# Optimization experiments

Hardware: AMD Instinct MI355X
Metric: run time of the kernel (lower is better)

The kernel has to match this reference:

```python
import jax, jax.numpy as jnp
import numpy as np

N_NODES = 50000
N_EDGES = 800000
IN_C, HID_C, OUT_C = 128, 128, 64


def setup_inputs() -> dict:
    key = jax.random.key(0)
    k1, k2, k3, k4 = jax.random.split(key, 4)
    x = jax.random.normal(k1, (N_NODES, IN_C), dtype=jnp.float32)
    edge_index = jax.random.randint(k2, (2, N_EDGES), 0, N_NODES, dtype=jnp.int64)
    # Glorot-ish init for weights, zero bias (PyG GCNConv default has bias)
    W1 = jax.random.normal(k3, (IN_C, HID_C), dtype=jnp.float32) * (1.0 / np.sqrt(IN_C))
    b1 = jnp.zeros((HID_C,), dtype=jnp.float32)
    W2 = jax.random.normal(k4, (HID_C, OUT_C), dtype=jnp.float32) * (1.0 / np.sqrt(HID_C))
    b2 = jnp.zeros((OUT_C,), dtype=jnp.float32)
    return {"x": x, "edge_index": edge_index, "W1": W1, "b1": b1, "W2": W2, "b2": b2}


def _gcn_norm(edge_index, num_nodes):
    """PyG gcn_norm: add self-loops, symmetric deg^{-1/2} normalization."""
    loop = jnp.arange(num_nodes, dtype=edge_index.dtype)
    src = jnp.concatenate([edge_index[0], loop])  # [E + N]
    dst = jnp.concatenate([edge_index[1], loop])
    ones = jnp.ones(src.shape[0], dtype=jnp.float32)
    deg = jax.ops.segment_sum(ones, dst, num_segments=num_nodes)  # in-degree incl. self-loop
    dinv = jnp.where(deg > 0, jax.lax.rsqrt(deg), 0.0)
    norm = dinv[src] * dinv[dst]  # [E + N]
    return src, dst, norm


def _gcn_conv(x, W, b, src, dst, norm, num_nodes):
    h = x @ W                                   # [N, C_out] transform first (PyG order)
    msg = h[src] * norm[:, None]                # gather + normalize, [E+N, C_out]
    out = jax.ops.segment_sum(msg, dst, num_segments=num_nodes)  # scatter-add
    return out + b


def reference(x, edge_index, W1, b1, W2, b2):
    N = x.shape[0]
    src, dst, norm = _gcn_norm(edge_index, N)  # graph normalization shared by both layers
    h = jax.nn.relu(_gcn_conv(x, W1, b1, src, dst, norm, N))
    out = _gcn_conv(h, W2, b2, src, dst, norm, N)
    return out
```

## Files before the change

### kernel.cpp

```cpp
#include <hip/hip_runtime.h>
#include <hip/hip_bf16.h>

#define IN_C  128
#define HID_C 128
#define OUT_CC 64
#define BK    128
#define CAPLG 12

using short8  = __attribute__((ext_vector_type(8))) short;
using float4v = __attribute__((ext_vector_type(4))) float;

__device__ __forceinline__ unsigned short f2b(float f) {
    unsigned int u = __float_as_uint(f);
    return (unsigned short)((u + 0x7fffu + ((u >> 16) & 1u)) >> 16);
}
__device__ __forceinline__ unsigned int pack2(float a, float b) {
    return (unsigned int)f2b(a) | ((unsigned int)f2b(b) << 16);
}
__device__ __forceinline__ float2 bf2_to_f2(unsigned int v) {
    float2 r;
    r.x = __uint_as_float(v << 16);
    r.y = __uint_as_float(v & 0xffff0000u);
    return r;
}


__global__ __launch_bounds__(256) void k_bpart(const int* __restrict__ ei,
                                               int* __restrict__ bfill,
                                               int* __restrict__ ebuf, int E, int NBK,
                                               int NCHK,
                                               const float* __restrict__ W1,
                                               const float* __restrict__ W2,
                                               unsigned short* __restrict__ w1f,
                                               unsigned short* __restrict__ w2f) {
    const int t = threadIdx.x;
    if ((int)blockIdx.x >= NCHK) {
        int e = ((int)blockIdx.x - NCHK) * 256 + t;
        if (e < 16384) {
            int j = e & 7, lane = (e >> 3) & 63, ks = (e >> 9) & 3, nt = e >> 11;
            int k = ks * 32 + ((lane >> 4) << 3) + j;
            int n = nt * 16 + (lane & 15);
            w1f[e] = f2b(W1[k * 128 + n]);
        } else if (e < 16384 + 8192) {
            int e2 = e - 16384;
            int j = e2 & 7, lane = (e2 >> 3) & 63, ks = (e2 >> 9) & 3, nt = e2 >> 11;
            int k = ks * 32 + ((lane >> 4) << 3) + j;
            int n = nt * 16 + (lane & 15);
            w2f[e2] = f2b(W2[k * 64 + n]);
        }
        return;
    }
    __shared__ int lh[512];
    __shared__ int lbase[512];
    __shared__ int s_st;
    for (int i = t; i < NBK; i += 256) lh[i] = 0;
    if (t < 64) {
        int ev = ei[2 * t], od = ei[2 * t + 1];
        unsigned long long onz = __ballot(od != 0);
        unsigned long long enz = __ballot(ev != 0);
        if (t == 0) s_st = (onz == 0ull && enz != 0ull) ? 2 : 1;
    }
    __syncthreads();
    const int st = s_st;
    const int base = blockIdx.x * 2048;
    int s[8], d[8];
    #pragma unroll
    for (int j = 0; j < 8; ++j) {
        int i = base + j * 256 + t;
        if (i < E) {
            s[j] = ei[(size_t)st * i];
            d[j] = ei[(size_t)st * ((size_t)E + i)];
            atomicAdd(&lh[d[j] >> 7], 1);
        } else d[j] = -1;
    }
    __syncthreads();
    for (int i = t; i < NBK; i += 256) {
        int c = lh[i];
        lbase[i] = c ? atomicAdd(&bfill[i], c) : 0;
        lh[i] = 0;
    }
    __syncthreads();
    #pragma unroll
    for (int j = 0; j < 8; ++j) {
        if (d[j] >= 0) {
            int b = d[j] >> 7;
            int r = lbase[b] + atomicAdd(&lh[b], 1);
            if (r < (1 << CAPLG))
                ebuf[(b << CAPLG) + r] = s[j] | ((d[j] & (BK - 1)) << 20);
        }
    }
}

__global__ __launch_bounds__(256) void k_blmg1(const int* __restrict__ ebuf,
                                               const int* __restrict__ bfill,
                                               int2* __restrict__ begend,
                                               float* __restrict__ dinv,
                                               int* __restrict__ col,
                                               const float* __restrict__ x,
                                               const unsigned short* __restrict__ w1f,
                                               unsigned short* __restrict__ h,
                                               int N, int NBK) {
    __shared__ unsigned short lds[64 * 136];
    __shared__ int cnt64[64];
    const int t = threadIdx.x;

    if ((int)blockIdx.x < NBK) {
        int* cnt = (int*)lds;
        int* sc  = cnt + BK;
        int* off = sc + BK;
        const int n0 = blockIdx.x * BK;
        const int beg = (int)blockIdx.x << CAPLG;
        const int ecnt = min(bfill[blockIdx.x], 1 << CAPLG);
        if (t < BK) cnt[t] = 0;
        __syncthreads();
        for (int i = t; i < ecnt; i += 256)
            atomicAdd(&cnt[ebuf[beg + i] >> 20], 1);
        __syncthreads();
        if (t < BK) sc[t] = cnt[t];
        __syncthreads();
        for (int o = 1; o < BK; o <<= 1) {
            int v = (t < BK && t >= o) ? sc[t - o] : 0;
            __syncthreads();
            if (t < BK) sc[t] += v;
            __syncthreads();
        }
        if (t < BK) {
            int c = cnt[t];
            off[t] = sc[t] - c;
            if (n0 + t < N) {
                begend[n0 + t] = make_int2(beg + off[t], beg + sc[t]);
                dinv[n0 + t] = rsqrtf((float)c + 1.0f);
            }
            cnt[t] = 0;
        }
        __syncthreads();
        for (int i = t; i < ecnt; i += 256) {
            int e = ebuf[beg + i];
            int dl = e >> 20;
            int p = beg + off[dl] + atomicAdd(&cnt[dl], 1);
            col[p] = e & 0xFFFFF;
        }
        return;
    }

    const int tile = (int)blockIdx.x - NBK;
    const int row0 = tile * 64;
    const int bkt  = row0 >> 7;
    const int half = (row0 >> 6) & 1;
    if (t < 64) cnt64[t] = 0;
    __syncthreads();
    {
        const int ebeg = bkt << CAPLG;
        const int ecnt = min(bfill[bkt], 1 << CAPLG);
        for (int i = t; i < ecnt; i += 256) {
            int dl = ebuf[ebeg + i] >> 20;
            if ((dl >> 6) == half) atomicAdd(&cnt64[dl & 63], 1);
        }
    }
    {
        int r = t >> 2, cc = (t & 3) * 32;
        int grow = row0 + r;
        unsigned int* dst = (unsigned int*)&lds[r * 136 + cc];
        if (grow < N) {
            const float4* src = (const float4*)(x + (size_t)grow * 128 + cc);
            #pragma unroll
            for (int i = 0; i < 8; ++i) {
                float4 v = src[i];
                dst[2 * i]     = pack2(v.x, v.y);
                dst[2 * i + 1] = pack2(v.z, v.w);
            }
        } else {
            #pragma unroll
            for (int i = 0; i < 16; ++i) dst[i] = 0;
        }
    }
    __syncthreads();
    const int w = t >> 6, lane = t & 63;
    const int quad = lane >> 4, m = lane & 15;
    short8 a[4];
    #pragma unroll
    for (int ks = 0; ks < 4; ++ks)
        a[ks] = *(const short8*)&lds[(w * 16 + m) * 136 + ks * 32 + quad * 8];
    float4v acc[8];
    #pragma unroll
    for (int nt = 0; nt < 8; ++nt) acc[nt] = (float4v){0.f, 0.f, 0.f, 0.f};
    const short8* wf = (const short8*)w1f;
    #pragma unroll
    for (int nt = 0; nt < 8; ++nt)
        #pragma unroll
        for (int ks = 0; ks < 4; ++ks)
            acc[nt] = __builtin_amdgcn_mfma_f32_16x16x32_bf16(a[ks], wf[(nt * 4 + ks) * 64 + lane],
                                                              acc[nt], 0, 0, 0);
    float drr[4];
    #pragma unroll
    for (int r = 0; r < 4; ++r) {
        int lr = w * 16 + quad * 4 + r;
        drr[r] = rsqrtf((float)cnt64[lr] + 1.0f);
    }
    #pragma unroll
    for (int nt = 0; nt < 8; ++nt)
        #pragma unroll
        for (int r = 0; r < 4; ++r) {
            int grow = row0 + w * 16 + quad * 4 + r;
            if (grow < N) h[(size_t)grow * 128 + nt * 16 + m] = f2b(acc[nt][r] * drr[r]);
        }
}

#define ACC16(u) { float2 q; \
    q = bf2_to_f2(u.x); a0 += q.x; a1 += q.y; \
    q = bf2_to_f2(u.y); a2 += q.x; a3 += q.y; \
    q = bf2_to_f2(u.z); a4 += q.x; a5 += q.y; \
    q = bf2_to_f2(u.w); a6 += q.x; a7 += q.y; }

#define PIPE_GATHER(FEATP, ROWSTRIDE, LANEOFF) \
    int c0, c1, c2, c3; \
    uint4 u0, u1, u2, u3; \
    { \
        int rem = end - e; \
        if (rem >= 4) { \
            c0 = col[e]; c1 = col[e + 1]; c2 = col[e + 2]; c3 = col[e + 3]; \
            u0 = FEATP[(size_t)c0 * ROWSTRIDE + LANEOFF]; \
            u1 = FEATP[(size_t)c1 * ROWSTRIDE + LANEOFF]; \
            u2 = FEATP[(size_t)c2 * ROWSTRIDE + LANEOFF]; \
            u3 = FEATP[(size_t)c3 * ROWSTRIDE + LANEOFF]; \
            if (rem >= 8) { c0 = col[e + 4]; c1 = col[e + 5]; c2 = col[e + 6]; c3 = col[e + 7]; } \
        } \
    } \
    for (; e + 12 <= end; e += 4) { \
        int n0 = col[e + 8], n1 = col[e + 9], n2 = col[e + 10], n3 = col[e + 11]; \
        uint4 v0 = FEATP[(size_t)c0 * ROWSTRIDE + LANEOFF]; \
        uint4 v1 = FEATP[(size_t)c1 * ROWSTRIDE + LANEOFF]; \
        uint4 v2 = FEATP[(size_t)c2 * ROWSTRIDE + LANEOFF]; \
        uint4 v3 = FEATP[(size_t)c3 * ROWSTRIDE + LANEOFF]; \
        ACC16(u0) ACC16(u1) ACC16(u2) ACC16(u3) \
        u0 = v0; u1 = v1; u2 = v2; u3 = v3; \
        c0 = n0; c1 = n1; c2 = n2; c3 = n3; \
    } \
    if (e + 8 <= end) { \
        uint4 v0 = FEATP[(size_t)c0 * ROWSTRIDE + LANEOFF]; \
        uint4 v1 = FEATP[(size_t)c1 * ROWSTRIDE + LANEOFF]; \
        uint4 v2 = FEATP[(size_t)c2 * ROWSTRIDE + LANEOFF]; \
        uint4 v3 = FEATP[(size_t)c3 * ROWSTRIDE + LANEOFF]; \
        ACC16(u0) ACC16(u1) ACC16(u2) ACC16(u3) \
        ACC16(v0) ACC16(v1) ACC16(v2) ACC16(v3) \
        e += 8; \
    } else if (e + 4 <= end) { \
        ACC16(u0) ACC16(u1) ACC16(u2) ACC16(u3) \
        e += 4; \
    } \
    for (; e < end; ++e) { \
        uint4 u = FEATP[(size_t)col[e] * ROWSTRIDE + LANEOFF]; \
        ACC16(u) \
    }

__global__ __launch_bounds__(256) void k_aggmg2(const uint4* __restrict__ feat,
                                                const int2* __restrict__ begend,
                                                const int* __restrict__ col,
                                                const float* __restrict__ dinv,
                                                const float* __restrict__ b1,
                                                const unsigned short* __restrict__ w2f,
                                                unsigned short* __restrict__ h2, int N) {
    __shared__ unsigned short lds[16 * 136];
    __shared__ float dvs[16];
    const int grp = threadIdx.x >> 4;
    const int l16 = threadIdx.x & 15;
    const int node = blockIdx.x * 16 + grp;
    float a0 = 0.f, a1 = 0.f, a2 = 0.f, a3 = 0.f, a4 = 0.f, a5 = 0.f, a6 = 0.f, a7 = 0.f;
    if (node < N) {
        const float dd = dinv[node];
        if (l16 == 0) dvs[grp] = dd;
        const int2 be = begend[node];
        int e = be.x; const int end = be.y;
        {
            uint4 sv = feat[(size_t)node * 16 + l16];
            float2 q;
            q = bf2_to_f2(sv.x); a0 = q.x; a1 = q.y;
            q = bf2_to_f2(sv.y); a2 = q.x; a3 = q.y;
            q = bf2_to_f2(sv.z); a4 = q.x; a5 = q.y;
            q = bf2_to_f2(sv.w); a6 = q.x; a7 = q.y;
        }
        PIPE_GATHER(feat, 16, l16)
        float4 ba = ((const float4*)b1)[2 * l16];
        float4 bb = ((const float4*)b1)[2 * l16 + 1];
        a0 = fmaxf(a0 * dd + ba.x, 0.0f);
        a1 = fmaxf(a1 * dd + ba.y, 0.0f);
        a2 = fmaxf(a2 * dd + ba.z, 0.0f);
        a3 = fmaxf(a3 * dd + ba.w, 0.0f);
        a4 = fmaxf(a4 * dd + bb.x, 0.0f);
        a5 = fmaxf(a5 * dd + bb.y, 0.0f);
        a6 = fmaxf(a6 * dd + bb.z, 0.0f);
        a7 = fmaxf(a7 * dd + bb.w, 0.0f);
    } else if (l16 == 0) dvs[grp] = 0.f;
    {
        uint4 o;
        o.x = pack2(a0, a1);
        o.y = pack2(a2, a3);
        o.z = pack2(a4, a5);
        o.w = pack2(a6, a7);
        *(uint4*)&lds[grp * 136 + l16 * 8] = o;
    }
    __syncthreads();
    const int w = threadIdx.x >> 6, lane = threadIdx.x & 63;
    const int quad = lane >> 4, m = lane & 15;
    short8 a[4];
    #pragma unroll
    for (int ks = 0; ks < 4; ++ks)
        a[ks] = *(const short8*)&lds[m * 136 + ks * 32 + quad * 8];
    float4v acc = (float4v){0.f, 0.f, 0.f, 0.f};
    const short8* wf = (const short8*)w2f;
    #pragma unroll
    for (int ks = 0; ks < 4; ++ks)
        acc = __builtin_amdgcn_mfma_f32_16x16x32_bf16(a[ks], wf[(w * 4 + ks) * 64 + lane],
                                                      acc, 0, 0, 0);
    const int node0 = blockIdx.x * 16;
    #pragma unroll
    for (int r = 0; r < 4; ++r) {
        int gn = node0 + quad * 4 + r;
        if (gn < N) h2[(size_t)gn * 64 + w * 16 + m] = f2b(acc[r] * dvs[quad * 4 + r]);
    }
}

__global__ __launch_bounds__(256) void k_agg64(const uint4* __restrict__ feat,
                                               const int2* __restrict__ begend,
                                               const int* __restrict__ col,
                                               const float* __restrict__ dinv,
                                               const float* __restrict__ bias,
                                               float* __restrict__ out, int N) {
    const int grp = threadIdx.x >> 3;
    const int l8  = threadIdx.x & 7;
    const int node = blockIdx.x * 32 + grp;
    if (node >= N) return;
    const float dd = dinv[node];
    const int2 be = begend[node];
    int e = be.x; const int end = be.y;
    float a0, a1, a2, a3, a4, a5, a6, a7;
    {
        uint4 sv = feat[(size_t)node * 8 + l8];
        float2 q;
        q = bf2_to_f2(sv.x); a0 = q.x; a1 = q.y;
        q = bf2_to_f2(sv.y); a2 = q.x; a3 = q.y;
        q = bf2_to_f2(sv.z); a4 = q.x; a5 = q.y;
        q = bf2_to_f2(sv.w); a6 = q.x; a7 = q.y;
    }
    PIPE_GATHER(feat, 8, l8)
    float4 ba = ((const float4*)bias)[2 * l8];
    float4 bb = ((const float4*)bias)[2 * l8 + 1];
    float4 o1, o2;
    o1.x = a0 * dd + ba.x;
    o1.y = a1 * dd + ba.y;
    o1.z = a2 * dd + ba.z;
    o1.w = a3 * dd + ba.w;
    o2.x = a4 * dd + bb.x;
    o2.y = a5 * dd + bb.y;
    o2.z = a6 * dd + bb.z;
    o2.w = a7 * dd + bb.w;
    float4* op = (float4*)out + (size_t)node * 16 + 2 * l8;
    op[0] = o1;
    op[1] = o2;
}

extern "C" void kernel_launch(void* const* d_in, const int* in_sizes, int n_in,
                              void* d_out, int out_size, void* d_ws, size_t ws_size,
                              hipStream_t stream) {
    const float* x  = (const float*)d_in[0];
    const int*   ei = (const int*)d_in[1];
    const float* W1 = (const float*)d_in[2];
    const float* b1 = (const float*)d_in[3];
    const float* W2 = (const float*)d_in[4];
    const float* b2 = (const float*)d_in[5];

    const int N = in_sizes[0] / IN_C;
    const int E = in_sizes[1] / 2;
    const int NBK  = (N + BK - 1) / BK;
    const int NCHK = (E + 2047) / 2048;
    const int NT1  = (N + 63) / 64;

    char* ws = (char*)d_ws;
    int*            bfill   = (int*)(ws + 64);
    int2*           begend  = (int2*)(ws + 4096);
    float*          dinv    = (float*)(ws + 404480);
    unsigned short* w1f     = (unsigned short*)(ws + 604672);
    unsigned short* w2f     = (unsigned short*)(ws + 637440);
    int*            ebuf    = (int*)(ws + 655360);
    int*            col     = (int*)(ws + 7061504);
    unsigned short* h       = (unsigned short*)(ws + 13467904);
    unsigned short* h2      = (unsigned short*)(ws + 26267904);

    hipMemsetAsync(bfill, 0, NBK * sizeof(int), stream);

    k_bpart<<<NCHK + 96, 256, 0, stream>>>(ei, bfill, ebuf, E, NBK, NCHK,
                                           W1, W2, w1f, w2f);

    k_blmg1<<<NBK + NT1, 256, 0, stream>>>(ebuf, bfill, begend, dinv, col,
                                           x, w1f, h, N, NBK);

    k_aggmg2<<<(N + 15) / 16, 256, 0, stream>>>((const uint4*)h, begend, col, dinv, b1,
                                                w2f, h2, N);

    k_agg64<<<(N + 31) / 32, 256, 0, stream>>>((const uint4*)h2, begend, col, dinv, b2,
                                               (float*)d_out, N);
}
```

Before: 164.3 us.

## Sort nodes by degree bucket to balance gather work across wavefront groups

Builds a degree histogram in the CSR build kernel, then a new kernel creates a permutation of nodes grouped by (capped) in-degree. Both aggregation kernels iterate nodes through this permutation, so the lanes of one wavefront handle nodes with similar edge counts and lose less time to divergent loop lengths. The gather macro is also simplified to a shallower software pipeline. This costs an extra launch, atomic-based binning, an indirect node lookup and scattered output writes, and row locality in h/h2 reads and writes is lost.

```diff
diff --git a/kernel.cpp b/kernel.cpp
--- a/kernel.cpp
+++ b/kernel.cpp
@@ -99,15 +99,17 @@
                                                const float* __restrict__ x,
                                                const unsigned short* __restrict__ w1f,
                                                unsigned short* __restrict__ h,
+                                               int* __restrict__ gbins,
                                                int N, int NBK) {
     __shared__ unsigned short lds[64 * 136];
     __shared__ int cnt64[64];
     const int t = threadIdx.x;
 
     if ((int)blockIdx.x < NBK) {
-        int* cnt = (int*)lds;
-        int* sc  = cnt + BK;
-        int* off = sc + BK;
+        int* cnt   = (int*)lds;
+        int* sc    = cnt + BK;
+        int* off   = sc + BK;
+        int* lbins = off + BK;
         const int n0 = blockIdx.x * BK;
         const int beg = (int)blockIdx.x << CAPLG;
         const int ecnt = min(bfill[blockIdx.x], 1 << CAPLG);
@@ -124,22 +126,28 @@
             if (t < BK) sc[t] += v;
             __syncthreads();
         }
+        int mydeg = -1;
         if (t < BK) {
             int c = cnt[t];
             off[t] = sc[t] - c;
             if (n0 + t < N) {
                 begend[n0 + t] = make_int2(beg + off[t], beg + sc[t]);
                 dinv[n0 + t] = rsqrtf((float)c + 1.0f);
+                mydeg = min(c, 63);
             }
             cnt[t] = 0;
         }
+        if (t >= 128 && t < 192) lbins[t - 128] = 0;
         __syncthreads();
+        if (mydeg >= 0) atomicAdd(&lbins[mydeg], 1);
         for (int i = t; i < ecnt; i += 256) {
             int e = ebuf[beg + i];
             int dl = e >> 20;
             int p = beg + off[dl] + atomicAdd(&cnt[dl], 1);
             col[p] = e & 0xFFFFF;
         }
+        __syncthreads();
+        if (t < 64 && lbins[t]) atomicAdd(&gbins[t], lbins[t]);
         return;
     }
 
@@ -206,6 +214,27 @@
         }
 }
 
+__global__ __launch_bounds__(128) void k_perm(const int2* __restrict__ begend,
+                                              const int* __restrict__ gbins,
+                                              int* __restrict__ binfill,
+                                              int* __restrict__ perm, int N) {
+    __shared__ int boff[64];
+    const int t = threadIdx.x;
+    if (t == 0) {
+        int s = 0;
+        #pragma unroll
+        for (int i = 0; i < 64; ++i) { int c = gbins[i]; boff[i] = s; s += c; }
+    }
+    __syncthreads();
+    int node = blockIdx.x * 128 + t;
+    if (node < N) {
+        int2 be = begend[node];
+        int dg = min(be.y - be.x, 63);
+        int r = boff[dg] + atomicAdd(&binfill[dg], 1);
+        perm[r] = node;
+    }
+}
+
 #define ACC16(u) { float2 q; \
     q = bf2_to_f2(u.x); a0 += q.x; a1 += q.y; \
     q = bf2_to_f2(u.y); a2 += q.x; a3 += q.y; \
@@ -214,37 +243,21 @@
 
 #define PIPE_GATHER(FEATP, ROWSTRIDE, LANEOFF) \
     int c0, c1, c2, c3; \
-    uint4 u0, u1, u2, u3; \
-    { \
-        int rem = end - e; \
-        if (rem >= 4) { \
-            c0 = col[e]; c1 = col[e + 1]; c2 = col[e + 2]; c3 = col[e + 3]; \
-            u0 = FEATP[(size_t)c0 * ROWSTRIDE + LANEOFF]; \
-            u1 = FEATP[(size_t)c1 * ROWSTRIDE + LANEOFF]; \
-            u2 = FEATP[(size_t)c2 * ROWSTRIDE + LANEOFF]; \
-            u3 = FEATP[(size_t)c3 * ROWSTRIDE + LANEOFF]; \
-            if (rem >= 8) { c0 = col[e + 4]; c1 = col[e + 5]; c2 = col[e + 6]; c3 = col[e + 7]; } \
-        } \
+    if (e + 4 <= end) { c0 = col[e]; c1 = col[e + 1]; c2 = col[e + 2]; c3 = col[e + 3]; } \
+    for (; e + 8 <= end; e += 4) { \
+        int p0 = col[e + 4], p1 = col[e + 5], p2 = col[e + 6], p3 = col[e + 7]; \
+        uint4 u0 = FEATP[(size_t)c0 * ROWSTRIDE + LANEOFF]; \
+        uint4 u1 = FEATP[(size_t)c1 * ROWSTRIDE + LANEOFF]; \
+        uint4 u2 = FEATP[(size_t)c2 * ROWSTRIDE + LANEOFF]; \
+        uint4 u3 = FEATP[(size_t)c3 * ROWSTRIDE + LANEOFF]; \
+        ACC16(u0) ACC16(u1) ACC16(u2) ACC16(u3) \
+        c0 = p0; c1 = p1; c2 = p2; c3 = p3; \
     } \
-    for (; e + 12 <= end; e += 4) { \
-        int n0 = col[e + 8], n1 = col[e + 9], n2 = col[e + 10], n3 = col[e + 11]; \
-        uint4 v0 = FEATP[(size_t)c0 * ROWSTRIDE + LANEOFF]; \
-        uint4 v1 = FEATP[(size_t)c1 * ROWSTRIDE + LANEOFF]; \
-        uint4 v2 = FEATP[(size_t)c2 * ROWSTRIDE + LANEOFF]; \
-        uint4 v3 = FEATP[(size_t)c3 * ROWSTRIDE + LANEOFF]; \
-        ACC16(u0) ACC16(u1) ACC16(u2) ACC16(u3) \
-        u0 = v0; u1 = v1; u2 = v2; u3 = v3; \
-        c0 = n0; c1 = n1; c2 = n2; c3 = n3; \
-    } \
-    if (e + 8 <= end) { \
-        uint4 v0 = FEATP[(size_t)c0 * ROWSTRIDE + LANEOFF]; \
-        uint4 v1 = FEATP[(size_t)c1 * ROWSTRIDE + LANEOFF]; \
-        uint4 v2 = FEATP[(size_t)c2 * ROWSTRIDE + LANEOFF]; \
-        uint4 v3 = FEATP[(size_t)c3 * ROWSTRIDE + LANEOFF]; \
-        ACC16(u0) ACC16(u1) ACC16(u2) ACC16(u3) \
-        ACC16(v0) ACC16(v1) ACC16(v2) ACC16(v3) \
-        e += 8; \
-    } else if (e + 4 <= end) { \
+    if (e + 4 <= end) { \
+        uint4 u0 = FEATP[(size_t)c0 * ROWSTRIDE + LANEOFF]; \
+        uint4 u1 = FEATP[(size_t)c1 * ROWSTRIDE + LANEOFF]; \
+        uint4 u2 = FEATP[(size_t)c2 * ROWSTRIDE + LANEOFF]; \
+        uint4 u3 = FEATP[(size_t)c3 * ROWSTRIDE + LANEOFF]; \
         ACC16(u0) ACC16(u1) ACC16(u2) ACC16(u3) \
         e += 4; \
     } \
@@ -259,16 +272,19 @@
                                                 const float* __restrict__ dinv,
                                                 const float* __restrict__ b1,
                                                 const unsigned short* __restrict__ w2f,
+                                                const int* __restrict__ perm,
                                                 unsigned short* __restrict__ h2, int N) {
     __shared__ unsigned short lds[16 * 136];
     __shared__ float dvs[16];
+    __shared__ int   pn[16];
     const int grp = threadIdx.x >> 4;
     const int l16 = threadIdx.x & 15;
-    const int node = blockIdx.x * 16 + grp;
+    const int slot = blockIdx.x * 16 + grp;
+    const int node = (slot < N) ? perm[slot] : -1;
     float a0 = 0.f, a1 = 0.f, a2 = 0.f, a3 = 0.f, a4 = 0.f, a5 = 0.f, a6 = 0.f, a7 = 0.f;
-    if (node < N) {
+    if (node >= 0) {
         const float dd = dinv[node];
-        if (l16 == 0) dvs[grp] = dd;
+        if (l16 == 0) { dvs[grp] = dd; pn[grp] = node; }
         const int2 be = begend[node];
         int e = be.x; const int end = be.y;
         {
@@ -290,7 +306,7 @@
         a5 = fmaxf(a5 * dd + bb.y, 0.0f);
         a6 = fmaxf(a6 * dd + bb.z, 0.0f);
         a7 = fmaxf(a7 * dd + bb.w, 0.0f);
-    } else if (l16 == 0) dvs[grp] = 0.f;
+    } else if (l16 == 0) { dvs[grp] = 0.f; pn[grp] = -1; }
     {
         uint4 o;
         o.x = pack2(a0, a1);
@@ -312,11 +328,10 @@
     for (int ks = 0; ks < 4; ++ks)
         acc = __builtin_amdgcn_mfma_f32_16x16x32_bf16(a[ks], wf[(w * 4 + ks) * 64 + lane],
                                                       acc, 0, 0, 0);
-    const int node0 = blockIdx.x * 16;
     #pragma unroll
     for (int r = 0; r < 4; ++r) {
-        int gn = node0 + quad * 4 + r;
-        if (gn < N) h2[(size_t)gn * 64 + w * 16 + m] = f2b(acc[r] * dvs[quad * 4 + r]);
+        int gn = pn[quad * 4 + r];
+        if (gn >= 0) h2[(size_t)gn * 64 + w * 16 + m] = f2b(acc[r] * dvs[quad * 4 + r]);
     }
 }
 
@@ -325,11 +340,13 @@
                                                const int* __restrict__ col,
                                                const float* __restrict__ dinv,
                                                const float* __restrict__ bias,
+                                               const int* __restrict__ perm,
                                                float* __restrict__ out, int N) {
     const int grp = threadIdx.x >> 3;
     const int l8  = threadIdx.x & 7;
-    const int node = blockIdx.x * 32 + grp;
-    if (node >= N) return;
+    const int slot = blockIdx.x * 32 + grp;
+    if (slot >= N) return;
+    const int node = perm[slot];
     const float dd = dinv[node];
     const int2 be = begend[node];
     int e = be.x; const int end = be.y;
@@ -374,9 +391,12 @@
     const int NBK  = (N + BK - 1) / BK;
     const int NCHK = (E + 2047) / 2048;
     const int NT1  = (N + 63) / 64;
+    const int NPB  = (N + 127) / 128;
 
     char* ws = (char*)d_ws;
     int*            bfill   = (int*)(ws + 64);
+    int*            gbins   = (int*)(ws + 1664);
+    int*            binfill = (int*)(ws + 1920);
     int2*           begend  = (int2*)(ws + 4096);
     float*          dinv    = (float*)(ws + 404480);
     unsigned short* w1f     = (unsigned short*)(ws + 604672);
@@ -385,18 +405,21 @@
     int*            col     = (int*)(ws + 7061504);
     unsigned short* h       = (unsigned short*)(ws + 13467904);
     unsigned short* h2      = (unsigned short*)(ws + 26267904);
-
-    hipMemsetAsync(bfill, 0, NBK * sizeof(int), stream);
+    int*            perm    = (int*)(ws + 32668160);
+
+    hipMemsetAsync(ws + 64, 0, 4032, stream);
 
     k_bpart<<<NCHK + 96, 256, 0, stream>>>(ei, bfill, ebuf, E, NBK, NCHK,
                                            W1, W2, w1f, w2f);
 
     k_blmg1<<<NBK + NT1, 256, 0, stream>>>(ebuf, bfill, begend, dinv, col,
-                                           x, w1f, h, N, NBK);
+                                           x, w1f, h, gbins, N, NBK);
+
+    k_perm<<<NPB, 128, 0, stream>>>(begend, gbins, binfill, perm, N);
 
     k_aggmg2<<<(N + 15) / 16, 256, 0, stream>>>((const uint4*)h, begend, col, dinv, b1,
-                                                w2f, h2, N);
+                                                w2f, perm, h2, N);
 
     k_agg64<<<(N + 31) / 32, 256, 0, stream>>>((const uint4*)h2, begend, col, dinv, b2,
-                                               (float*)d_out, N);
-}
+                                               perm, (float*)d_out, N);
+}
```

Result: slower. 295.4 us (+79.8%).
